# Performance work log

Hardware: AMD Instinct MI355X
Metric: run time of the kernel (lower is better)

## Reference

```python
import jax, jax.numpy as jnp
import numpy as np
import math

T = 2048; HID = 2048; H = 16; KV = 8; G = H // KV; D = 128
GH = 128; BS = 64; NB = T // BS
EPS = 1e-6; RATIO = 0.2; SCALE = 1.0 / math.sqrt(D)


def _rope_tables(length, dim, theta=1000000.0):
    inv = 1.0 / (theta ** (np.arange(0, dim, 2, dtype=np.float32) / dim))
    f = np.outer(np.arange(length, dtype=np.float32), inv)
    emb = np.concatenate([f, f], axis=-1)
    return jnp.asarray(np.cos(emb)), jnp.asarray(np.sin(emb))


def _rot_half(x):
    d = x.shape[-1] // 2
    return jnp.concatenate([-x[..., d:], x[..., :d]], axis=-1)


def _apply_rope(x, cos, sin):
    # x: [T, nH, D], cos/sin: [T, D] broadcast over head dim
    return x * cos[:, None, :] + _rot_half(x) * sin[:, None, :]


def _rmsnorm(x, w, eps=EPS):
    xf = x.astype(jnp.float32)
    v = jnp.mean(xf * xf, axis=-1, keepdims=True)
    return (w * (xf * jax.lax.rsqrt(v + eps))).astype(x.dtype)


def setup_inputs() -> dict:
    key = jax.random.key(0)
    ks = jax.random.split(key, 8)
    s = 0.02
    hidden_states = jax.random.normal(ks[0], (T, HID), jnp.float32)
    Wq = jax.random.normal(ks[1], (HID, H * D), jnp.float32) * s
    Wk = jax.random.normal(ks[2], (HID, KV * D), jnp.float32) * s
    Wv = jax.random.normal(ks[3], (HID, KV * D), jnp.float32) * s
    Wo = jax.random.normal(ks[4], (H * D, HID), jnp.float32) * s
    q_norm_w = jnp.ones((D,), jnp.float32)
    k_norm_w = jnp.ones((D,), jnp.float32)
    gate_wq = jax.random.normal(ks[5], (D, GH), jnp.float32) * s
    gate_wk = jax.random.normal(ks[6], (D, GH), jnp.float32) * s
    cos, sin = _rope_tables(T, D)
    cos_gq, sin_gq = _rope_tables(T, GH)
    cos_blk, sin_blk = _rope_tables(NB, GH)
    # causal block mask: query t may attend to key block j iff j <= t // BS
    block_attention_mask = (jnp.arange(T)[:, None] // BS) >= jnp.arange(NB)[None, :]
    return dict(hidden_states=hidden_states, Wq=Wq, Wk=Wk, Wv=Wv, Wo=Wo,
                q_norm_w=q_norm_w, k_norm_w=k_norm_w, gate_wq=gate_wq, gate_wk=gate_wk,
                cos=cos, sin=sin, cos_gq=cos_gq, sin_gq=sin_gq,
                cos_blk=cos_blk, sin_blk=sin_blk,
                block_attention_mask=block_attention_mask)


def reference(hidden_states, Wq, Wk, Wv, Wo, q_norm_w, k_norm_w, gate_wq, gate_wk,
              cos, sin, cos_gq, sin_gq, cos_blk, sin_blk, block_attention_mask):
    q = (hidden_states @ Wq).reshape(T, H, D)
    k = (hidden_states @ Wk).reshape(T, KV, D)
    v = (hidden_states @ Wv).reshape(T, KV, D)
    q = _rmsnorm(q, q_norm_w)
    k = _rmsnorm(k, k_norm_w)

    # ---- gate network on un-roped q/k: q-head avg-pool to KV heads, k avg-pool per block ----
    q_pool = q.reshape(T, KV, G, D).mean(axis=2)            # [T, KV, D]
    gq = _apply_rope(q_pool @ gate_wq, cos_gq, sin_gq)      # [T, KV, GH]
    k_blk = k.reshape(NB, BS, KV, D).mean(axis=1)           # [NB, KV, D]
    gk = _apply_rope(k_blk @ gate_wk, cos_blk, sin_blk)     # [NB, KV, GH]
    gate_scores = jnp.einsum('tkg,nkg->ktn', gq, gk) / math.sqrt(GH)  # [KV, T, NB]
    predict_mask = jnp.where(block_attention_mask[None], gate_scores, -1e9)

    # ---- main attention (RoPE + GQA causal softmax attention) ----
    qr = _apply_rope(q, cos, sin)
    kr = _apply_rope(k, cos, sin)
    kr_rep = jnp.repeat(kr, G, axis=1)                      # [T, H, D]
    v_rep = jnp.repeat(v, G, axis=1)
    logits = jnp.einsum('thd,shd->hts', qr, kr_rep) * SCALE  # [H, T, T]
    causal = jnp.tril(jnp.ones((T, T), bool))
    logits = jnp.where(causal[None], logits, -jnp.inf)
    probs = jax.nn.softmax(logits, axis=-1)
    attn_output = jnp.einsum('hts,shd->thd', probs, v_rep).reshape(T, H * D) @ Wo

    # ---- pooled ground-truth block mask: attention mass per key block ----
    pooled = probs.reshape(H, T, NB, BS).sum(axis=-1)        # [H, T, NB]
    gt = pooled.reshape(KV, G, T, NB).max(axis=1)            # max_pool3d over head groups -> [KV,T,NB]
    gt = jnp.where(block_attention_mask[None], gt, 0.0)
    gt = gt / (gt.sum(axis=-1, keepdims=True) + 1e-9)

    # ---- KLDiv gate loss on the tail slice (bsz = 1) ----
    start = int(T * RATIO)
    tgt = gt[:, start:, :]                                   # [KV, L, NB]
    logp = jax.nn.log_softmax(predict_mask[:, start:, :], axis=-1)
    safe_t = jnp.where(tgt > 0, tgt, 1.0)
    kl = jnp.where(tgt > 0, tgt * (jnp.log(safe_t) - logp), 0.0)
    gate_loss = kl.reshape(KV, -1).mean(axis=-1).sum()       # KLDivLoss(reduction='mean') per kv head, summed, /bsz(=1)
    return attn_output, gate_loss
```

## Files before the change

### kernel.cpp

```cpp
#include <hip/hip_runtime.h>

#define T_ 2048
#define HID_ 2048
#define H_ 16
#define KV_ 8
#define G_ 2
#define D_ 128
#define GH_ 128
#define BS_ 64
#define NB_ 32
#define START_ 409
#define TG0_ 384
#define SCALE_ 0.08838834764831845f
#define MFIX_ 8.0f

typedef __attribute__((ext_vector_type(8))) short short8_t;
typedef __attribute__((ext_vector_type(4))) float float4_t;
typedef __attribute__((ext_vector_type(8))) unsigned short ushort8_t;
typedef __attribute__((ext_vector_type(4))) unsigned short ushort4_t;

__device__ __forceinline__ float wave_sum(float v) {
#pragma unroll
  for (int o = 32; o > 0; o >>= 1) v += __shfl_xor(v, o, 64);
  return v;
}
__device__ __forceinline__ unsigned short f2bf(float x) {
  unsigned int u = __float_as_uint(x);
  unsigned int r = (u + 0x7fffu + ((u >> 16) & 1u)) >> 16;
  return (unsigned short)r;
}

__device__ __forceinline__ void gload16(const void* g, void* l) {
  __builtin_amdgcn_global_load_lds((const __attribute__((address_space(1))) unsigned int*)g,
                                   (__attribute__((address_space(3))) unsigned int*)l, 16, 0, 0);
}

__device__ __forceinline__ void castT_dev(const float* __restrict__ in,
                                          unsigned short* __restrict__ out, int K, int N,
                                          int ldin, int bx, int by,
                                          unsigned short (*tile)[72], int tid) {
  int k0 = by * 64, n0 = bx * 64;
  int tx = tid & 63, ty4 = tid >> 6;
#pragma unroll
  for (int i = 0; i < 16; ++i) {
    int ky = ty4 * 16 + i;
    tile[tx][ky] = f2bf(in[(size_t)(k0 + ky) * ldin + n0 + tx]);
  }
  __syncthreads();
#pragma unroll
  for (int i = 0; i < 16; ++i) {
    int ny = ty4 * 16 + i;
    out[(size_t)(n0 + ny) * K + k0 + tx] = tile[ny][tx];
  }
}

__global__ __launch_bounds__(256) void castT(const float* __restrict__ in,
                                             unsigned short* __restrict__ out,
                                             int K, int N, int ldin) {
  __shared__ unsigned short tile[64][72];
  castT_dev(in, out, K, N, ldin, blockIdx.x, blockIdx.y, tile, threadIdx.x);
}

__global__ __launch_bounds__(256) void prep_cast(const float* __restrict__ hs,
                                                 const float* __restrict__ Wq,
                                                 const float* __restrict__ Wk,
                                                 const float* __restrict__ Wv,
                                                 const float* __restrict__ Wo,
                                                 const float* __restrict__ gwq,
                                                 const float* __restrict__ gwk,
                                                 unsigned short* __restrict__ hsb,
                                                 unsigned short* __restrict__ WqkvT,
                                                 unsigned short* __restrict__ WoT,
                                                 unsigned short* __restrict__ gwqT,
                                                 unsigned short* __restrict__ gwkT) {
  __shared__ unsigned short tile[64][72];
  int id = blockIdx.x, tid = threadIdx.x;
  if (id < 4096) {
    int i = id * 256 + tid;
    float4 v = ((const float4*)hs)[i];
    ushort4_t o = {f2bf(v.x), f2bf(v.y), f2bf(v.z), f2bf(v.w)};
    *(ushort4_t*)(hsb + (size_t)i * 4) = o;
  } else if (id < 5120) {
    int t = id - 4096;
    castT_dev(Wq, WqkvT, 2048, 2048, 2048, t & 31, t >> 5, tile, tid);
  } else if (id < 5632) {
    int t = id - 5120;
    castT_dev(Wk, WqkvT + (size_t)2048 * 2048, 2048, 1024, 1024, t & 15, t >> 4, tile, tid);
  } else if (id < 6144) {
    int t = id - 5632;
    castT_dev(Wv, WqkvT + (size_t)3072 * 2048, 2048, 1024, 1024, t & 15, t >> 4, tile, tid);
  } else if (id < 7168) {
    int t = id - 6144;
    castT_dev(Wo, WoT, 2048, 2048, 2048, t & 31, t >> 5, tile, tid);
  } else if (id < 7172) {
    int t = id - 7168;
    castT_dev(gwq, gwqT, 128, 128, 128, t & 1, t >> 1, tile, tid);
  } else {
    int t = id - 7172;
    castT_dev(gwk, gwkT, 128, 128, 128, t & 1, t >> 1, tile, tid);
  }
}

__device__ __forceinline__ void gemm_body(const unsigned short* __restrict__ A,
                                          const unsigned short* __restrict__ Bt,
                                          float* __restrict__ C,
                                          int M, int N, int K, int ldc, int bx, int by,
                                          unsigned short* As, unsigned short* Bs) {
  int tid = threadIdx.x;
  int wid = tid >> 6, lane = tid & 63;
  int quad = lane >> 4, l16 = lane & 15;
  int wm = wid & 1, wn = wid >> 1;
  int m0 = by * 128, n0 = bx * 128;
  const unsigned short* gA[4];
  const unsigned short* gB[4];
#pragma unroll
  for (int it = 0; it < 4; ++it) {
    int line = wid * 32 + it * 8 + (lane >> 3);
    int chunk = (lane & 7) ^ (line & 7);
    gA[it] = A + (size_t)(m0 + line) * K + chunk * 8;
    gB[it] = Bt + (size_t)(n0 + line) * K + chunk * 8;
  }
  float4_t acc[4][4];
#pragma unroll
  for (int i = 0; i < 4; ++i)
#pragma unroll
    for (int j = 0; j < 4; ++j) acc[i][j] = (float4_t){0.f, 0.f, 0.f, 0.f};
  for (int k0 = 0; k0 < K; k0 += 64) {
    __syncthreads();
#pragma unroll
    for (int it = 0; it < 4; ++it) {
      gload16(gA[it] + k0, As + (wid * 32 + it * 8) * 64);
      gload16(gB[it] + k0, Bs + (wid * 32 + it * 8) * 64);
    }
    __syncthreads();
    short8_t a[2][4], b[2][4];
#pragma unroll
    for (int ks = 0; ks < 2; ++ks) {
      int sw = ((ks * 4 + quad) ^ (l16 & 7)) * 8;
#pragma unroll
      for (int i = 0; i < 4; ++i) {
        a[ks][i] = *(const short8_t*)&As[(wm * 64 + i * 16 + l16) * 64 + sw];
        b[ks][i] = *(const short8_t*)&Bs[(wn * 64 + i * 16 + l16) * 64 + sw];
      }
    }
#pragma unroll
    for (int ks = 0; ks < 2; ++ks)
#pragma unroll
      for (int i = 0; i < 4; ++i)
#pragma unroll
        for (int j = 0; j < 4; ++j)
          acc[i][j] = __builtin_amdgcn_mfma_f32_16x16x32_bf16(a[ks][i], b[ks][j], acc[i][j], 0, 0, 0);
  }
#pragma unroll
  for (int i = 0; i < 4; ++i)
#pragma unroll
    for (int j = 0; j < 4; ++j)
#pragma unroll
      for (int reg = 0; reg < 4; ++reg)
        C[(size_t)(m0 + wm * 64 + i * 16 + quad * 4 + reg) * ldc + n0 + wn * 64 + j * 16 + l16] =
            acc[i][j][reg];
}

__global__ __launch_bounds__(256) void gemm_bf16_v3(const unsigned short* __restrict__ A,
                                                    const unsigned short* __restrict__ Bt,
                                                    float* __restrict__ C,
                                                    int M, int N, int K, int ldc) {
  __shared__ unsigned short As[128 * 64];
  __shared__ unsigned short Bs[128 * 64];
  gemm_body(A, Bt, C, M, N, K, ldc, blockIdx.x, blockIdx.y, As, Bs);
}

__global__ __launch_bounds__(256) void gemm_gates(const unsigned short* __restrict__ Aq,
                                                  const unsigned short* __restrict__ Bq,
                                                  float* __restrict__ Cq,
                                                  const unsigned short* __restrict__ Ak,
                                                  const unsigned short* __restrict__ Bk,
                                                  float* __restrict__ Ck) {
  __shared__ unsigned short As[128 * 64];
  __shared__ unsigned short Bs[128 * 64];
  int y = blockIdx.y;
  if (y < 104)
    gemm_body(Aq, Bq, Cq, 13312, 128, 128, 128, 0, y, As, Bs);
  else
    gemm_body(Ak, Bk, Ck, 256, 128, 128, 128, 0, y - 104, As, Bs);
}

__global__ __launch_bounds__(128) void norm_rope_fused(const float* __restrict__ qkvf,
                                                       const float* __restrict__ qw,
                                                       const float* __restrict__ kw,
                                                       const float* __restrict__ cosT,
                                                       const float* __restrict__ sinT,
                                                       unsigned short* __restrict__ qbf,
                                                       unsigned short* __restrict__ qpool_bf,
                                                       unsigned short* __restrict__ kbf,
                                                       float* __restrict__ knorm) {
  int t = blockIdx.x, d = threadIdx.x;
  if (blockIdx.y < 8) {
    int kv = blockIdx.y;
    size_t i0 = (size_t)t * 4096 + (kv * G_) * D_ + d;
    float x0 = qkvf[i0], x1 = qkvf[i0 + D_];
    __shared__ float sred[2][2];
    float s0 = wave_sum(x0 * x0), s1 = wave_sum(x1 * x1);
    if ((d & 63) == 0) { sred[0][d >> 6] = s0; sred[1][d >> 6] = s1; }
    __syncthreads();
    float wv = qw[d];
    float n0 = x0 * rsqrtf((sred[0][0] + sred[0][1]) * (1.f / D_) + 1e-6f) * wv;
    float n1 = x1 * rsqrtf((sred[1][0] + sred[1][1]) * (1.f / D_) + 1e-6f) * wv;
    if (t >= TG0_) qpool_bf[((size_t)(t - TG0_) * KV_ + kv) * D_ + d] = f2bf(0.5f * (n0 + n1));
    __shared__ float sh[2][D_];
    sh[0][d] = n0; sh[1][d] = n1;
    __syncthreads();
    float c = cosT[t * D_ + d], s = sinT[t * D_ + d];
    float r0 = (d < 64) ? -sh[0][d + 64] : sh[0][d - 64];
    float r1 = (d < 64) ? -sh[1][d + 64] : sh[1][d - 64];
    qbf[((size_t)(t * H_) + kv * G_) * D_ + d] = f2bf(n0 * c + r0 * s);
    qbf[((size_t)(t * H_) + kv * G_ + 1) * D_ + d] = f2bf(n1 * c + r1 * s);
  } else {
    int kv = blockIdx.y - 8;
    float x = qkvf[(size_t)t * 4096 + 2048 + kv * D_ + d];
    __shared__ float sredk[2];
    float s0 = wave_sum(x * x);
    if ((d & 63) == 0) sredk[d >> 6] = s0;
    __syncthreads();
    float nk = x * rsqrtf((sredk[0] + sredk[1]) * (1.f / D_) + 1e-6f) * kw[d];
    knorm[(size_t)(t * KV_ + kv) * D_ + d] = nk;
    __shared__ float shk[D_];
    shk[d] = nk;
    __syncthreads();
    float rot = (d < 64) ? -shk[d + 64] : shk[d - 64];
    kbf[(size_t)(t * KV_ + kv) * D_ + d] = f2bf(nk * cosT[t * D_ + d] + rot * sinT[t * D_ + d]);
  }
}

__global__ __launch_bounds__(128) void kblk_kernel(const float* __restrict__ knorm,
                                                   unsigned short* __restrict__ kblk_bf) {
  int n = blockIdx.x, kv = blockIdx.y, d = threadIdx.x;
  float s = 0.f;
  for (int i = 0; i < BS_; ++i) s += knorm[((size_t)(n * BS_ + i) * KV_ + kv) * D_ + d];
  kblk_bf[(size_t)(n * KV_ + kv) * D_ + d] = f2bf(s * (1.f / BS_));
}

__global__ __launch_bounds__(128) void rope_g_fused(float* __restrict__ gq, float* __restrict__ gk,
                                                    const float* __restrict__ cosG,
                                                    const float* __restrict__ sinG,
                                                    const float* __restrict__ cosB,
                                                    const float* __restrict__ sinB) {
  int r = blockIdx.x, kvh = blockIdx.y, d = threadIdx.x;
  float* x;
  size_t base;
  float c_, s_;
  if (r < NB_) {
    x = gk;
    base = (size_t)(r * KV_ + kvh) * GH_;
    c_ = cosB[r * GH_ + d]; s_ = sinB[r * GH_ + d];
  } else {
    int rr = r - NB_;
    x = gq;
    base = (size_t)(rr * KV_ + kvh) * GH_;
    c_ = cosG[(size_t)(TG0_ + rr) * GH_ + d]; s_ = sinG[(size_t)(TG0_ + rr) * GH_ + d];
  }
  __shared__ float sh[GH_];
  sh[d] = x[base + d];
  __syncthreads();
  float rot = (d < 64) ? -sh[d + 64] : sh[d - 64];
  x[base + d] = sh[d] * c_ + rot * s_;
}

__global__ __launch_bounds__(256, 2) void attn_mfma(const unsigned short* __restrict__ qbf,
                                                    const unsigned short* __restrict__ kbf,
                                                    const unsigned short* __restrict__ vt,
                                                    float* __restrict__ pooled,
                                                    float* __restrict__ o_acc,
                                                    float* __restrict__ l_acc) {
  int kv = blockIdx.x;
  int yy = blockIdx.y;
  int tile, c_lo, c_hi;
  if (yy < 32) { tile = yy;      c_lo = 0;                c_hi = (tile + 2) >> 1; }
  else         { tile = 63 - yy; c_lo = (tile + 2) >> 1;  c_hi = tile + 1; }
  int t0 = tile * 64;
  int tid = threadIdx.x;
  int wid = tid >> 6, lane = tid & 63;
  int quad = lane >> 4, l16 = lane & 15;
  __shared__ unsigned short Ks[2][64 * 128];
  __shared__ unsigned short Vs[2][128 * 64];
  __shared__ unsigned short Ps[8][16 * 64];

  const unsigned short* kbase[4];
  const unsigned short* vbase[4];
#pragma unroll
  for (int it = 0; it < 4; ++it) {
    int seg = wid * 4 + it;
    int krow = seg * 4 + (lane >> 4);
    int kchk = lane & 15;
    kbase[it] = kbf + ((size_t)krow * KV_ + kv) * D_ + ((kchk ^ (krow & 7)) << 3);
    int vrow = seg * 8 + (lane >> 3);
    int vchk = lane & 7;
    vbase[it] = vt + (size_t)(kv * 128 + vrow) * T_ + ((vchk ^ (vrow & 7)) << 3);
  }

  int tq = t0 + wid * 16 + l16;
  short8_t qf[2][4];
#pragma unroll
  for (int hh = 0; hh < 2; ++hh)
#pragma unroll
    for (int kb = 0; kb < 4; ++kb)
      qf[hh][kb] = *(const short8_t*)&qbf[((size_t)tq * H_ + kv * G_ + hh) * D_ + kb * 32 + quad * 8];

  const short one_bf = (short)0x3F80;
  short8_t ones = {one_bf, one_bf, one_bf, one_bf, one_bf, one_bf, one_bf, one_bf};

  int tbase = t0 + wid * 16 + quad * 4;
  float l_[2][4] = {};
  float pacc[2][2][4] = {};
  float4_t o[2][8];
#pragma unroll
  for (int hh = 0; hh < 2; ++hh)
#pragma unroll
    for (int j = 0; j < 8; ++j) o[hh][j] = (float4_t){0.f, 0.f, 0.f, 0.f};

#pragma unroll
  for (int it = 0; it < 4; ++it) {
    gload16(kbase[it] + (size_t)c_lo * 65536, &Ks[c_lo & 1][(wid * 4 + it) * 512]);
    gload16(vbase[it] + c_lo * 64, &Vs[c_lo & 1][(wid * 4 + it) * 512]);
  }
  for (int c = c_lo; c < c_hi; ++c) {
    __syncthreads();
    if (c + 1 < c_hi) {
      int b = (c + 1) & 1;
#pragma unroll
      for (int it = 0; it < 4; ++it) {
        gload16(kbase[it] + (size_t)(c + 1) * 65536, &Ks[b][(wid * 4 + it) * 512]);
        gload16(vbase[it] + (c + 1) * 64, &Vs[b][(wid * 4 + it) * 512]);
      }
    }
    const unsigned short* Ksc = Ks[c & 1];
    const unsigned short* Vsc = Vs[c & 1];
    int half = c >> 4, cl = c & 15;

    float4_t s[2][4];
#pragma unroll
    for (int j = 0; j < 4; ++j) {
      float4_t a0 = (float4_t){0.f, 0.f, 0.f, 0.f};
      float4_t a1 = (float4_t){0.f, 0.f, 0.f, 0.f};
#pragma unroll
      for (int kb = 0; kb < 4; ++kb) {
        short8_t kf = *(const short8_t*)&Ksc[(j * 16 + l16) * 128 + (((kb * 4 + quad) ^ (l16 & 7)) << 3)];
        a0 = __builtin_amdgcn_mfma_f32_16x16x32_bf16(qf[0][kb], kf, a0, 0, 0, 0);
        a1 = __builtin_amdgcn_mfma_f32_16x16x32_bf16(qf[1][kb], kf, a1, 0, 0, 0);
      }
      s[0][j] = a0;
      s[1][j] = a1;
    }
#pragma unroll
    for (int hh = 0; hh < 2; ++hh) {
      if (c == tile) {
#pragma unroll
        for (int reg = 0; reg < 4; ++reg) {
          int trow = tbase + reg;
#pragma unroll
          for (int j = 0; j < 4; ++j) {
            float p = __expf(s[hh][j][reg] * SCALE_ - MFIX_);
            s[hh][j][reg] = (c * 64 + j * 16 + l16 <= trow) ? p : 0.f;
          }
        }
      } else {
#pragma unroll
        for (int j = 0; j < 4; ++j)
#pragma unroll
          for (int reg = 0; reg < 4; ++reg)
            s[hh][j][reg] = __expf(s[hh][j][reg] * SCALE_ - MFIX_);
      }
#pragma unroll
      for (int j = 0; j < 4; ++j)
#pragma unroll
        for (int reg = 0; reg < 4; ++reg) {
          int r = quad * 4 + reg;
          Ps[wid * 2 + hh][r * 64 + ((j * 16 + l16) ^ ((r & 7) << 3))] = f2bf(s[hh][j][reg]);
        }
    }
    float4_t pool[2] = {(float4_t){0.f, 0.f, 0.f, 0.f}, (float4_t){0.f, 0.f, 0.f, 0.f}};
#pragma unroll
    for (int ks = 0; ks < 2; ++ks) {
      int psw = l16 * 64 + (((ks * 4 + quad) ^ (l16 & 7)) << 3);
      short8_t pf0 = *(const short8_t*)&Ps[wid * 2 + 0][psw];
      short8_t pf1 = *(const short8_t*)&Ps[wid * 2 + 1][psw];
      pool[0] = __builtin_amdgcn_mfma_f32_16x16x32_bf16(pf0, ones, pool[0], 0, 0, 0);
      pool[1] = __builtin_amdgcn_mfma_f32_16x16x32_bf16(pf1, ones, pool[1], 0, 0, 0);
#pragma unroll
      for (int jt = 0; jt < 8; ++jt) {
        short8_t vf = *(const short8_t*)&Vsc[(jt * 16 + l16) * 64 + (((ks * 4 + quad) ^ (l16 & 7)) << 3)];
        o[0][jt] = __builtin_amdgcn_mfma_f32_16x16x32_bf16(pf0, vf, o[0][jt], 0, 0, 0);
        o[1][jt] = __builtin_amdgcn_mfma_f32_16x16x32_bf16(pf1, vf, o[1][jt], 0, 0, 0);
      }
    }
#pragma unroll
    for (int hh = 0; hh < 2; ++hh)
#pragma unroll
      for (int reg = 0; reg < 4; ++reg) {
        l_[hh][reg] += pool[hh][reg];
        if (l16 == cl) pacc[hh][half][reg] = pool[hh][reg];
      }
  }
#pragma unroll
  for (int hh = 0; hh < 2; ++hh) {
    int h = kv * G_ + hh;
#pragma unroll
    for (int reg = 0; reg < 4; ++reg) {
      int trow = tbase + reg;
      if (l16 >= c_lo && l16 < c_hi)
        pooled[((size_t)h * T_ + trow) * NB_ + l16] = pacc[hh][0][reg];
      if (16 + l16 >= c_lo && 16 + l16 < c_hi)
        pooled[((size_t)h * T_ + trow) * NB_ + 16 + l16] = pacc[hh][1][reg];
    }
#pragma unroll
    for (int jt = 0; jt < 8; ++jt)
#pragma unroll
      for (int reg = 0; reg < 4; ++reg)
        atomicAdd(&o_acc[(((size_t)h * T_) + tbase + reg) * D_ + jt * 16 + l16], o[hh][jt][reg]);
    if (l16 == 0) {
#pragma unroll
      for (int reg = 0; reg < 4; ++reg)
        atomicAdd(&l_acc[(size_t)h * T_ + tbase + reg], l_[hh][reg]);
    }
  }
}

__global__ __launch_bounds__(256) void attn_combine(const float* __restrict__ o_acc,
                                                    const float* __restrict__ l_acc,
                                                    unsigned short* __restrict__ attnb) {
  int gid = blockIdx.x * 256 + threadIdx.x;
  int row = gid >> 5, q4 = gid & 31;
  int h = row >> 11, t = row & 2047;
  float inv = 1.f / l_acc[row];
  float4 a = ((const float4*)o_acc)[gid];
  ushort4_t ov = {f2bf(a.x * inv), f2bf(a.y * inv), f2bf(a.z * inv), f2bf(a.w * inv)};
  *(ushort4_t*)(attnb + (size_t)t * (H_ * D_) + h * D_ + q4 * 4) = ov;
}

__global__ __launch_bounds__(256) void gate_loss2(const float* __restrict__ gq,
                                                  const float* __restrict__ gk,
                                                  const float* __restrict__ pooled,
                                                  const float* __restrict__ l_acc,
                                                  float* __restrict__ klsum) {
  int kv = blockIdx.x;
  int sub = threadIdx.x >> 5;
  int n = threadIdx.x & 31;
  int tloc = blockIdx.y * 8 + sub;
  bool act = tloc < (T_ - START_);
  int t = START_ + (act ? tloc : 0);
  const float4* a = (const float4*)(gq + ((size_t)(t - TG0_) * KV_ + kv) * GH_);
  const float4* b = (const float4*)(gk + (size_t)(n * KV_ + kv) * GH_);
  float dot = 0.f;
#pragma unroll
  for (int d4 = 0; d4 < 32; ++d4) {
    float4 av = a[d4], bv = b[d4];
    dot += av.x * bv.x + av.y * bv.y + av.z * bv.z + av.w * bv.w;
  }
  bool valid = (t / BS_) >= n;
  float score = valid ? dot * SCALE_ : -1e9f;
  float M = score;
#pragma unroll
  for (int o = 16; o > 0; o >>= 1) M = fmaxf(M, __shfl_xor(M, o, 64));
  float e = __expf(score - M);
  float Z = e;
#pragma unroll
  for (int o = 16; o > 0; o >>= 1) Z += __shfl_xor(Z, o, 64);
  float logZ = M + logf(Z);
  float g = 0.f;
  if (valid) {
    float rl0 = 1.f / l_acc[(size_t)(kv * G_) * T_ + t];
    float rl1 = 1.f / l_acc[(size_t)(kv * G_ + 1) * T_ + t];
    float p0 = pooled[((size_t)(kv * G_) * T_ + t) * NB_ + n] * rl0;
    float p1 = pooled[((size_t)(kv * G_ + 1) * T_ + t) * NB_ + n] * rl1;
    g = fmaxf(p0, p1);
  }
  float gs = g;
#pragma unroll
  for (int o = 16; o > 0; o >>= 1) gs += __shfl_xor(gs, o, 64);
  float tgt = g / (gs + 1e-9f);
  float kl = (tgt > 0.f) ? tgt * (logf(tgt) - (score - logZ)) : 0.f;
  float ks = kl;
#pragma unroll
  for (int o = 16; o > 0; o >>= 1) ks += __shfl_xor(ks, o, 64);
  if (n == 0 && act) klsum[kv * (T_ - START_) + tloc] = ks;
}

__global__ __launch_bounds__(256) void finalize_loss(const float* __restrict__ klsum,
                                                     float* __restrict__ out) {
  const int n = KV_ * (T_ - START_);
  float s = 0.f;
  for (int i = threadIdx.x; i < n; i += 256) s += klsum[i];
  s = wave_sum(s);
  __shared__ float sh[4];
  if ((threadIdx.x & 63) == 0) sh[threadIdx.x >> 6] = s;
  __syncthreads();
  if (threadIdx.x == 0)
    out[0] = (sh[0] + sh[1] + sh[2] + sh[3]) * (1.f / ((float)(T_ - START_) * NB_));
}

extern "C" void kernel_launch(void* const* d_in, const int* in_sizes, int n_in,
                              void* d_out, int out_size, void* d_ws, size_t ws_size,
                              hipStream_t stream) {
  const float* hs   = (const float*)d_in[0];
  const float* Wq   = (const float*)d_in[1];
  const float* Wk   = (const float*)d_in[2];
  const float* Wv   = (const float*)d_in[3];
  const float* Wo   = (const float*)d_in[4];
  const float* qw   = (const float*)d_in[5];
  const float* kw   = (const float*)d_in[6];
  const float* gwq  = (const float*)d_in[7];
  const float* gwk  = (const float*)d_in[8];
  const float* cosT = (const float*)d_in[9];
  const float* sinT = (const float*)d_in[10];
  const float* cosG = (const float*)d_in[11];
  const float* sinG = (const float*)d_in[12];
  const float* cosB = (const float*)d_in[13];
  const float* sinB = (const float*)d_in[14];
  float* out = (float*)d_out;
  float* ws = (float*)d_ws;
  const size_t MEG = 1048576;

  float*          qkvf     = ws;
  unsigned short* attnb    = (unsigned short*)ws;
  float*          pooled   = ws + 2 * MEG;
  float*          klsum    = ws + 3 * MEG;
  float*          l_acc    = ws + 3 * MEG + 65536;
  float*          o_acc    = ws + 4 * MEG;
  unsigned short* WqkvT    = (unsigned short*)(ws + 8 * MEG);
  unsigned short* qbf      = WqkvT;
  unsigned short* kbf      = WqkvT + 4 * MEG;
  unsigned short* vt       = WqkvT + 6 * MEG;
  unsigned short* hsb      = (unsigned short*)(ws + 12 * MEG);
  float*          knorm    = ws + 12 * MEG;
  unsigned short* WoT      = (unsigned short*)(ws + 14 * MEG);
  unsigned short* qpool_bf = (unsigned short*)(ws + 16 * MEG);
  float*          gq       = ws + 17 * MEG;
  unsigned short* kblk_bf  = (unsigned short*)(ws + 18 * MEG + 786432);
  float*          gk       = ws + 18 * MEG + 819200;
  unsigned short* gwqT     = (unsigned short*)(ws + 18 * MEG + 851968);
  unsigned short* gwkT     = (unsigned short*)(ws + 18 * MEG + 860160);

  prep_cast<<<7176, 256, 0, stream>>>(hs, Wq, Wk, Wv, Wo, gwq, gwk, hsb, WqkvT, WoT, gwqT, gwkT);
  gemm_bf16_v3<<<dim3(32, 16), 256, 0, stream>>>(hsb, WqkvT, qkvf, 2048, 4096, 2048, 4096);
  norm_rope_fused<<<dim3(T_, 16), 128, 0, stream>>>(qkvf, qw, kw, cosT, sinT, qbf, qpool_bf,
                                                    kbf, knorm);
  castT<<<dim3(16, 32), 256, 0, stream>>>(qkvf + 3072, vt, T_, 1024, 4096);
  hipMemsetAsync(o_acc, 0, (size_t)4 * MEG * sizeof(float), stream);
  hipMemsetAsync(l_acc, 0, (size_t)H_ * T_ * sizeof(float), stream);
  kblk_kernel<<<dim3(NB_, KV_), 128, 0, stream>>>(knorm, kblk_bf);
  gemm_gates<<<dim3(1, 106), 256, 0, stream>>>(qpool_bf, gwqT, gq, kblk_bf, gwkT, gk);
  rope_g_fused<<<dim3(NB_ + (T_ - TG0_), KV_), 128, 0, stream>>>(gq, gk, cosG, sinG, cosB, sinB);
  attn_mfma<<<dim3(KV_, 64), 256, 0, stream>>>(qbf, kbf, vt, pooled, o_acc, l_acc);
  attn_combine<<<4096, 256, 0, stream>>>(o_acc, l_acc, attnb);
  gemm_bf16_v3<<<dim3(16, 16), 256, 0, stream>>>(attnb, WoT, out, 2048, 2048, 2048, 2048);
  gate_loss2<<<dim3(KV_, 205), 256, 0, stream>>>(gq, gk, pooled, l_acc, klsum);
  finalize_loss<<<1, 256, 0, stream>>>(klsum, out + (size_t)T_ * HID_);
}
```

Baseline: 358.0 us.

## Double-buffer GEMM LDS tiles and merge Wo GEMM with gate-loss launch

The shared bf16 GEMM body now uses two LDS buffers, so the global-to-LDS loads for the next K tile are issued before the current tile's MFMAs and one barrier per iteration is dropped. The Wo projection GEMM and the gate KL-loss kernel are merged into a single launch, with extra blocks running the gate-loss body. This saves a launch and lets the small gate work fill the GPU while the GEMM tiles run. In exchange LDS per block doubles to 64 KB, which may reduce occupancy. A single barrier per iteration may also allow overwriting a buffer still being read, if the loads are asynchronous.

```diff
diff --git a/kernel.cpp b/kernel.cpp
--- a/kernel.cpp
+++ b/kernel.cpp
@@ -125,22 +125,32 @@
   for (int i = 0; i < 4; ++i)
 #pragma unroll
     for (int j = 0; j < 4; ++j) acc[i][j] = (float4_t){0.f, 0.f, 0.f, 0.f};
-  for (int k0 = 0; k0 < K; k0 += 64) {
+  int nk = K >> 6;
+#pragma unroll
+  for (int it = 0; it < 4; ++it) {
+    gload16(gA[it], As + (wid * 32 + it * 8) * 64);
+    gload16(gB[it], Bs + (wid * 32 + it * 8) * 64);
+  }
+  for (int t = 0; t < nk; ++t) {
     __syncthreads();
-#pragma unroll
-    for (int it = 0; it < 4; ++it) {
-      gload16(gA[it] + k0, As + (wid * 32 + it * 8) * 64);
-      gload16(gB[it] + k0, Bs + (wid * 32 + it * 8) * 64);
-    }
-    __syncthreads();
+    if (t + 1 < nk) {
+      int bo = ((t + 1) & 1) * 8192;
+#pragma unroll
+      for (int it = 0; it < 4; ++it) {
+        gload16(gA[it] + (t + 1) * 64, As + bo + (wid * 32 + it * 8) * 64);
+        gload16(gB[it] + (t + 1) * 64, Bs + bo + (wid * 32 + it * 8) * 64);
+      }
+    }
+    const unsigned short* Asc = As + (t & 1) * 8192;
+    const unsigned short* Bsc = Bs + (t & 1) * 8192;
     short8_t a[2][4], b[2][4];
 #pragma unroll
     for (int ks = 0; ks < 2; ++ks) {
       int sw = ((ks * 4 + quad) ^ (l16 & 7)) * 8;
 #pragma unroll
       for (int i = 0; i < 4; ++i) {
-        a[ks][i] = *(const short8_t*)&As[(wm * 64 + i * 16 + l16) * 64 + sw];
-        b[ks][i] = *(const short8_t*)&Bs[(wn * 64 + i * 16 + l16) * 64 + sw];
+        a[ks][i] = *(const short8_t*)&Asc[(wm * 64 + i * 16 + l16) * 64 + sw];
+        b[ks][i] = *(const short8_t*)&Bsc[(wn * 64 + i * 16 + l16) * 64 + sw];
       }
     }
 #pragma unroll
@@ -165,8 +175,8 @@
                                                     const unsigned short* __restrict__ Bt,
                                                     float* __restrict__ C,
                                                     int M, int N, int K, int ldc) {
-  __shared__ unsigned short As[128 * 64];
-  __shared__ unsigned short Bs[128 * 64];
+  __shared__ unsigned short As[2 * 128 * 64];
+  __shared__ unsigned short Bs[2 * 128 * 64];
   gemm_body(A, Bt, C, M, N, K, ldc, blockIdx.x, blockIdx.y, As, Bs);
 }
 
@@ -176,8 +186,8 @@
                                                   const unsigned short* __restrict__ Ak,
                                                   const unsigned short* __restrict__ Bk,
                                                   float* __restrict__ Ck) {
-  __shared__ unsigned short As[128 * 64];
-  __shared__ unsigned short Bs[128 * 64];
+  __shared__ unsigned short As[2 * 128 * 64];
+  __shared__ unsigned short Bs[2 * 128 * 64];
   int y = blockIdx.y;
   if (y < 104)
     gemm_body(Aq, Bq, Cq, 13312, 128, 128, 128, 0, y, As, Bs);
@@ -437,15 +447,15 @@
   *(ushort4_t*)(attnb + (size_t)t * (H_ * D_) + h * D_ + q4 * 4) = ov;
 }
 
-__global__ __launch_bounds__(256) void gate_loss2(const float* __restrict__ gq,
-                                                  const float* __restrict__ gk,
-                                                  const float* __restrict__ pooled,
-                                                  const float* __restrict__ l_acc,
-                                                  float* __restrict__ klsum) {
-  int kv = blockIdx.x;
+__device__ __forceinline__ void gate_loss_body(const float* __restrict__ gq,
+                                               const float* __restrict__ gk,
+                                               const float* __restrict__ pooled,
+                                               const float* __restrict__ l_acc,
+                                               float* __restrict__ klsum,
+                                               int kv, int yblk) {
   int sub = threadIdx.x >> 5;
   int n = threadIdx.x & 31;
-  int tloc = blockIdx.y * 8 + sub;
+  int tloc = yblk * 8 + sub;
   bool act = tloc < (T_ - START_);
   int t = START_ + (act ? tloc : 0);
   const float4* a = (const float4*)(gq + ((size_t)(t - TG0_) * KV_ + kv) * GH_);
@@ -483,6 +493,25 @@
 #pragma unroll
   for (int o = 16; o > 0; o >>= 1) ks += __shfl_xor(ks, o, 64);
   if (n == 0 && act) klsum[kv * (T_ - START_) + tloc] = ks;
+}
+
+__global__ __launch_bounds__(256) void wo_gemm_gate(const unsigned short* __restrict__ A,
+                                                    const unsigned short* __restrict__ Bt,
+                                                    float* __restrict__ C,
+                                                    const float* __restrict__ gq,
+                                                    const float* __restrict__ gk,
+                                                    const float* __restrict__ pooled,
+                                                    const float* __restrict__ l_acc,
+                                                    float* __restrict__ klsum) {
+  __shared__ unsigned short As[2 * 128 * 64];
+  __shared__ unsigned short Bs[2 * 128 * 64];
+  if (blockIdx.y < 16) {
+    gemm_body(A, Bt, C, 2048, 2048, 2048, 2048, blockIdx.x, blockIdx.y, As, Bs);
+  } else {
+    int g = blockIdx.x + (blockIdx.y - 16) * 16;
+    int kv = g & 7, yblk = g >> 3;
+    if (yblk < 205) gate_loss_body(gq, gk, pooled, l_acc, klsum, kv, yblk);
+  }
 }
 
 __global__ __launch_bounds__(256) void finalize_loss(const float* __restrict__ klsum,
@@ -552,7 +581,6 @@
   rope_g_fused<<<dim3(NB_ + (T_ - TG0_), KV_), 128, 0, stream>>>(gq, gk, cosG, sinG, cosB, sinB);
   attn_mfma<<<dim3(KV_, 64), 256, 0, stream>>>(qbf, kbf, vt, pooled, o_acc, l_acc);
   attn_combine<<<4096, 256, 0, stream>>>(o_acc, l_acc, attnb);
-  gemm_bf16_v3<<<dim3(16, 16), 256, 0, stream>>>(attnb, WoT, out, 2048, 2048, 2048, 2048);
-  gate_loss2<<<dim3(KV_, 205), 256, 0, stream>>>(gq, gk, pooled, l_acc, klsum);
+  wo_gemm_gate<<<dim3(16, 119), 256, 0, stream>>>(attnb, WoT, out, gq, gk, pooled, l_acc, klsum);
   finalize_loss<<<1, 256, 0, stream>>>(klsum, out + (size_t)T_ * HID_);
 }
```

Result: faster. 333.1 us (-6.9%).
